# Performance work log

Hardware: AMD Instinct MI355X
Metric: run time of the kernel (lower is better)

The kernel has to match this reference:

```python
import jax, jax.numpy as jnp
import numpy as np

N_NODES = 100000
DROP_P = 0.2


def _degree_norm(idx, n):
    deg = jax.ops.segment_sum(jnp.ones_like(idx, dtype=jnp.float32), idx, num_segments=n)
    return jnp.maximum(deg, 1.0) ** -0.5


def gcn_layer(x, src, dst, W, b, n):
    # DGL GraphConv, norm='both', in_feats > out_feats so weight is applied first.
    norm_src = _degree_norm(src, n)  # out-degree^{-1/2}
    norm_dst = _degree_norm(dst, n)  # in-degree^{-1/2}
    h = (x * norm_src[:, None]) @ W            # [N, d_out]
    agg = jax.ops.segment_sum(h[src], dst, num_segments=n)  # gather-scatter over edges
    return agg * norm_dst[:, None] + b


def setup_inputs() -> dict:
    key = jax.random.key(0)
    k = jax.random.split(key, 5)
    x = jax.random.normal(k[0], (N_NODES, 256), dtype=jnp.float32)
    edge_index = jax.random.randint(k[1], (2, 1600000), 0, N_NODES, dtype=jnp.int64)
    W1 = jax.random.normal(k[2], (256, 128), dtype=jnp.float32) * (1.0 / np.sqrt(256))
    b1 = jnp.zeros((128,), dtype=jnp.float32)
    W2 = jax.random.normal(k[3], (128, 47), dtype=jnp.float32) * (1.0 / np.sqrt(128))
    b2 = jnp.zeros((47,), dtype=jnp.float32)
    return {"x": x, "edge_index": edge_index, "W1": W1, "b1": b1, "W2": W2, "b2": b2}


def reference(x, edge_index, W1, b1, W2, b2):
    src, dst = edge_index[0], edge_index[1]
    n = x.shape[0]
    # CRD: GraphConv -> relu -> dropout (F.dropout default training=True; fixed mask)
    h = gcn_layer(x, src, dst, W1, b1, n)
    h = jax.nn.relu(h)
    keep = jax.random.bernoulli(jax.random.key(42), 1.0 - DROP_P, h.shape)
    h = jnp.where(keep, h / (1.0 - DROP_P), 0.0)
    # CLS: GraphConv -> log_softmax over class dim
    out = gcn_layer(h, src, dst, W2, b2, n)
    return jax.nn.log_softmax(out, axis=-1)
```

## Files before the change

### kernel.cpp

```cpp
#include <hip/hip_runtime.h>
#include <math.h>


#define NF0 256
#define NF1 128
#define NC  47
#define CB  1024

typedef __attribute__((ext_vector_type(8))) short bfrag;
typedef __attribute__((ext_vector_type(4))) float f32x4;

__device__ __forceinline__ unsigned short f2bf(float f) {
  unsigned u = __float_as_uint(f);
  return (unsigned short)((u + 0x7fffu + ((u >> 16) & 1u)) >> 16);
}
__device__ __forceinline__ unsigned pack2bf(float a, float b) {
  return (unsigned)f2bf(a) | ((unsigned)f2bf(b) << 16);
}
__device__ __forceinline__ float bflo(unsigned v) { return __uint_as_float(v << 16); }
__device__ __forceinline__ float bfhi(unsigned v) { return __uint_as_float(v & 0xffff0000u); }
__device__ __forceinline__ float bf2f(unsigned short b) {
  return __uint_as_float((unsigned)b << 16);
}

__device__ __forceinline__ unsigned rotl_(unsigned x, int n) {
  return (x << n) | (x >> (32 - n));
}
__device__ __forceinline__ void threefry2x32_(unsigned x0, unsigned x1,
                                              unsigned& o0, unsigned& o1) {
  const unsigned k0 = 0u, k1 = 42u;
  const unsigned k2 = k0 ^ k1 ^ 0x1BD11BDAu;
  x0 += k0; x1 += k1;
  x0+=x1; x1=rotl_(x1,13); x1^=x0;
  x0+=x1; x1=rotl_(x1,15); x1^=x0;
  x0+=x1; x1=rotl_(x1,26); x1^=x0;
  x0+=x1; x1=rotl_(x1, 6); x1^=x0;
  x0+=k1; x1+=k2+1u;
  x0+=x1; x1=rotl_(x1,17); x1^=x0;
  x0+=x1; x1=rotl_(x1,29); x1^=x0;
  x0+=x1; x1=rotl_(x1,16); x1^=x0;
  x0+=x1; x1=rotl_(x1,24); x1^=x0;
  x0+=k2; x1+=k0+2u;
  x0+=x1; x1=rotl_(x1,13); x1^=x0;
  x0+=x1; x1=rotl_(x1,15); x1^=x0;
  x0+=x1; x1=rotl_(x1,26); x1^=x0;
  x0+=x1; x1=rotl_(x1, 6); x1^=x0;
  x0+=k0; x1+=k1+3u;
  x0+=x1; x1=rotl_(x1,17); x1^=x0;
  x0+=x1; x1=rotl_(x1,29); x1^=x0;
  x0+=x1; x1=rotl_(x1,16); x1^=x0;
  x0+=x1; x1=rotl_(x1,24); x1^=x0;
  x0+=k1; x1+=k2+4u;
  x0+=x1; x1=rotl_(x1,13); x1^=x0;
  x0+=x1; x1=rotl_(x1,15); x1^=x0;
  x0+=x1; x1=rotl_(x1,26); x1^=x0;
  x0+=x1; x1=rotl_(x1, 6); x1^=x0;
  x0+=k2; x1+=k0+5u;
  o0 = x0; o1 = x1;
}
__device__ __forceinline__ unsigned dropout_bit(unsigned j) {
  unsigned o0, o1;
  threefry2x32_(0u, j, o0, o1);
  unsigned bits = o0 ^ o1;
  float u = __uint_as_float((bits >> 9) | 0x3f800000u) - 1.0f;
  return (u < 0.8f) ? 1u : 0u;
}


__global__ __launch_bounds__(256) void k_chist(const int* __restrict__ ei, int E,
                                               int nbk,
                                               unsigned* __restrict__ bCntD,
                                               unsigned* __restrict__ bCntS,
                                               const float* __restrict__ W1,
                                               const float* __restrict__ W2,
                                               unsigned* __restrict__ W1t32,
                                               unsigned* __restrict__ W2t32) {
  if (blockIdx.x >= 256) {
    int i = (blockIdx.x - 256) * 256 + threadIdx.x;
    if (i < 128 * 128) {
      int n = i >> 7, k = (i & 127) << 1;
      W1t32[i] = pack2bf(W1[(size_t)k * NF1 + n], W1[(size_t)(k + 1) * NF1 + n]);
    } else if (i < 128 * 128 + 48 * 64) {
      int j = i - 128 * 128;
      int f = j >> 6, k = (j & 63) << 1;
      float a = (f < NC) ? W2[(size_t)k * NC + f] : 0.f;
      float c = (f < NC) ? W2[(size_t)(k + 1) * NC + f] : 0.f;
      W2t32[j] = pack2bf(a, c);
    }
    return;
  }
  __shared__ unsigned hd[128], hs[128];
  for (int i = threadIdx.x; i < 128; i += 256) { hd[i] = 0; hs[i] = 0; }
  __syncthreads();
  for (int e = blockIdx.x * 256 + threadIdx.x; e < E; e += 256 * 256) {
    int s = ei[e], d = ei[E + e];
    atomicAdd(&hs[s >> 10], 1u);
    atomicAdd(&hd[d >> 10], 1u);
  }
  __syncthreads();
  for (int i = threadIdx.x; i < nbk; i += 256) {
    if (hd[i]) atomicAdd(&bCntD[i], hd[i]);
    if (hs[i]) atomicAdd(&bCntS[i], hs[i]);
  }
}

__global__ __launch_bounds__(256) void k_cscatter(const int* __restrict__ ei, int E,
                                                  const unsigned* __restrict__ bCntD,
                                                  const unsigned* __restrict__ bCntS,
                                                  unsigned* __restrict__ curD,
                                                  unsigned* __restrict__ curS,
                                                  unsigned* __restrict__ pd,
                                                  unsigned short* __restrict__ ps,
                                                  int nbk) {
  __shared__ unsigned hd[128], hs[128];
  __shared__ unsigned baseD[128], baseS[128];
  __shared__ unsigned sc[256];
  const int t = threadIdx.x;
  int per = (E + gridDim.x - 1) / gridDim.x;
  int e0 = blockIdx.x * per;
  int e1 = min(e0 + per, E);
  unsigned orig = (t < 128) ? ((t < nbk) ? bCntD[t] : 0u)
                            : (((t - 128) < nbk) ? bCntS[t - 128] : 0u);
  sc[t] = orig;
  if (t < 128) { hd[t] = 0; hs[t] = 0; }
  __syncthreads();
  for (int e = e0 + t; e < e1; e += 256) {
    int s = ei[e], d = ei[E + e];
    atomicAdd(&hs[s >> 10], 1u);
    atomicAdd(&hd[d >> 10], 1u);
  }
  __syncthreads();
  #pragma unroll
  for (int o = 1; o < 128; o <<= 1) {
    unsigned u = ((t & 127) >= o) ? sc[t - o] : 0u;
    __syncthreads();
    sc[t] += u;
    __syncthreads();
  }
  if (t < 128) {
    unsigned excl = sc[t] - orig;
    unsigned h = hd[t];
    baseD[t] = excl + (h ? atomicAdd(&curD[t], h) : 0u);
    hd[t] = 0;
  } else {
    int i = t - 128;
    unsigned excl = sc[t] - orig;
    unsigned h = hs[i];
    baseS[i] = excl + (h ? atomicAdd(&curS[i], h) : 0u);
    hs[i] = 0;
  }
  __syncthreads();
  for (int e = e0 + t; e < e1; e += 256) {
    int s = ei[e], d = ei[E + e];
    int bd = d >> 10, bs = s >> 10;
    unsigned pD = baseD[bd] + atomicAdd(&hd[bd], 1u);
    unsigned pS = baseS[bs] + atomicAdd(&hs[bs], 1u);
    pd[pD] = ((unsigned)(d & (CB - 1)) << 17) | (unsigned)s;
    ps[pS] = (unsigned short)(s & (CB - 1));
  }
}

__global__ __launch_bounds__(256) void k_fine(const unsigned* __restrict__ bCntD,
                                              const unsigned* __restrict__ bCntS,
                                              const unsigned* __restrict__ pd,
                                              const unsigned short* __restrict__ ps,
                                              unsigned* __restrict__ off,
                                              float* __restrict__ norm_dst,
                                              float* __restrict__ norm_src,
                                              int* __restrict__ csr,
                                              int N, int E, int nbk,
                                              unsigned* __restrict__ bmask) {
  const int t = threadIdx.x;
  if ((int)blockIdx.x >= 2 * nbk) {
    int i = ((int)blockIdx.x - 2 * nbk) * 256 + t;
    if (i < 4 * N) {
      unsigned w = 0;
      #pragma unroll 4
      for (int tbit = 0; tbit < 32; tbit++)
        w |= dropout_bit(32u * (unsigned)i + (unsigned)tbit) << tbit;
      bmask[i] = w;
    }
    return;
  }
  __shared__ unsigned cnt[CB];
  __shared__ unsigned part[256];
  __shared__ unsigned sc[256];
  const bool isD = (int)blockIdx.x < nbk;
  const int b = isD ? (int)blockIdx.x : ((int)blockIdx.x - nbk);
  unsigned orig = (t < 128) ? ((t < nbk) ? bCntD[t] : 0u)
                            : (((t - 128) < nbk) ? bCntS[t - 128] : 0u);
  sc[t] = orig;
  __syncthreads();
  #pragma unroll
  for (int o = 1; o < 128; o <<= 1) {
    unsigned u = ((t & 127) >= o) ? sc[t - o] : 0u;
    __syncthreads();
    sc[t] += u;
    __syncthreads();
  }
  const int idx = isD ? b : (128 + b);
  const unsigned hi = sc[idx];
  const unsigned lo = hi - (isD ? bCntD[b] : bCntS[b]);
  const int base = b << 10;
  for (int i = t; i < CB; i += 256) cnt[i] = 0;
  __syncthreads();
  if (isD) {
    for (unsigned j = lo + t; j < hi; j += 256) atomicAdd(&cnt[pd[j] >> 17], 1u);
    __syncthreads();
    unsigned c0 = cnt[4*t], c1 = cnt[4*t+1], c2 = cnt[4*t+2], c3 = cnt[4*t+3];
    unsigned tsum = c0 + c1 + c2 + c3;
    part[t] = tsum;
    __syncthreads();
    #pragma unroll
    for (int o = 1; o < 256; o <<= 1) {
      unsigned u = (t >= o) ? part[t - o] : 0u;
      __syncthreads();
      part[t] += u;
      __syncthreads();
    }
    unsigned e0 = part[t] - tsum;
    unsigned p0 = e0, p1 = e0 + c0, p2 = p1 + c1, p3 = p2 + c2;
    int n0 = base + 4 * t;
    if (n0 + 0 < N) { off[n0+0] = lo + p0; norm_dst[n0+0] = 1.0f / sqrtf((float)(c0 < 1u ? 1u : c0)); }
    if (n0 + 1 < N) { off[n0+1] = lo + p1; norm_dst[n0+1] = 1.0f / sqrtf((float)(c1 < 1u ? 1u : c1)); }
    if (n0 + 2 < N) { off[n0+2] = lo + p2; norm_dst[n0+2] = 1.0f / sqrtf((float)(c2 < 1u ? 1u : c2)); }
    if (n0 + 3 < N) { off[n0+3] = lo + p3; norm_dst[n0+3] = 1.0f / sqrtf((float)(c3 < 1u ? 1u : c3)); }
    if (b == nbk - 1 && t == 0) off[N] = (unsigned)E;
    __syncthreads();
    cnt[4*t] = p0; cnt[4*t+1] = p1; cnt[4*t+2] = p2; cnt[4*t+3] = p3;
    __syncthreads();
    for (unsigned j = lo + t; j < hi; j += 256) {
      unsigned v = pd[j];
      unsigned pos = atomicAdd(&cnt[v >> 17], 1u);
      csr[lo + pos] = (int)(v & 0x1FFFFu);
    }
  } else {
    for (unsigned j = lo + t; j < hi; j += 256) atomicAdd(&cnt[ps[j]], 1u);
    __syncthreads();
    for (int i = t; i < CB; i += 256) {
      int n = base + i;
      if (n < N) {
        unsigned c = cnt[i];
        norm_src[n] = 1.0f / sqrtf((float)(c < 1u ? 1u : c));
      }
    }
  }
}

__global__ __launch_bounds__(256) void k_gemm1(const float* __restrict__ x,
                                               const unsigned* __restrict__ W1t32,
                                               const float* __restrict__ norm_src,
                                               unsigned short* __restrict__ h1, int N) {
  __shared__ unsigned As[128][20];
  __shared__ unsigned Bs[128][20];
  const int m0 = blockIdx.x * 128;
  const int t = threadIdx.x;
  const int lane = t & 63, wid = t >> 6;
  const int fr = lane & 15, ko = (lane >> 4) * 8;

  f32x4 acc[2][8];
  #pragma unroll
  for (int r = 0; r < 2; r++)
    #pragma unroll
    for (int c = 0; c < 8; c++) acc[r][c] = (f32x4){0.f, 0.f, 0.f, 0.f};

  const int sr = t >> 1;
  const int shw = (t & 1) * 8;

  for (int k0 = 0; k0 < NF0; k0 += 32) {
    {
      unsigned w[8];
      int gm = m0 + sr;
      if (gm < N) {
        const float* p = x + (size_t)gm * NF0 + k0 + shw * 2;
        #pragma unroll
        for (int q = 0; q < 4; q++) {
          float4 v = *(const float4*)(p + q * 4);
          w[2*q]   = pack2bf(v.x, v.y);
          w[2*q+1] = pack2bf(v.z, v.w);
        }
      } else {
        #pragma unroll
        for (int q = 0; q < 8; q++) w[q] = 0u;
      }
      *(uint4*)&As[sr][shw]     = make_uint4(w[0], w[1], w[2], w[3]);
      *(uint4*)&As[sr][shw + 4] = make_uint4(w[4], w[5], w[6], w[7]);
    }
    {
      const unsigned* pb = W1t32 + (size_t)sr * (NF0 / 2) + (k0 >> 1) + shw;
      *(uint4*)&Bs[sr][shw]     = *(const uint4*)pb;
      *(uint4*)&Bs[sr][shw + 4] = *(const uint4*)(pb + 4);
    }
    __syncthreads();
    const unsigned short* As16 = (const unsigned short*)&As[0][0];
    const unsigned short* Bs16 = (const unsigned short*)&Bs[0][0];
    #pragma unroll
    for (int r = 0; r < 2; r++) {
      bfrag a = *(const bfrag*)(As16 + (size_t)(wid * 32 + r * 16 + fr) * 40 + ko);
      #pragma unroll
      for (int c = 0; c < 8; c++) {
        bfrag b = *(const bfrag*)(Bs16 + (size_t)(c * 16 + fr) * 40 + ko);
        acc[r][c] = __builtin_amdgcn_mfma_f32_16x16x32_bf16(a, b, acc[r][c], 0, 0, 0);
      }
    }
    __syncthreads();
  }

  #pragma unroll
  for (int r = 0; r < 2; r++) {
    int rbase = m0 + wid * 32 + r * 16 + (lane >> 4) * 4;
    float ns[4];
    #pragma unroll
    for (int g = 0; g < 4; g++) ns[g] = (rbase + g < N) ? norm_src[rbase + g] : 0.f;
    #pragma unroll
    for (int c = 0; c < 8; c++) {
      int col = c * 16 + fr;
      #pragma unroll
      for (int g = 0; g < 4; g++) {
        int row = rbase + g;
        if (row < N) h1[(size_t)row * NF1 + col] = f2bf(acc[r][c][g] * ns[g]);
      }
    }
  }
}

__global__ __launch_bounds__(256) void k_gather1(const unsigned* __restrict__ off,
                                                 const int* __restrict__ csr,
                                                 const unsigned short* __restrict__ h1,
                                                 const float* __restrict__ norm_dst,
                                                 const float* __restrict__ norm_src,
                                                 const float* __restrict__ b1,
                                                 const unsigned* __restrict__ bmask,
                                                 const unsigned* __restrict__ W2t32,
                                                 unsigned short* __restrict__ g64,
                                                 int N) {
  const int t = threadIdx.x;
  const int lane = t & 63, wid = t >> 6;
  const int eg = lane >> 4;
  const int q  = lane & 15;
  const float4 bA = *(const float4*)(b1 + q * 8);
  const float4 bB = *(const float4*)(b1 + q * 8 + 4);

  const int wbase = (blockIdx.x * 4 + wid) * 16;
  if (wbase >= N) return;

  uint4 af[4];
  #pragma unroll
  for (int kk = 0; kk < 4; kk++) af[kk] = make_uint4(0u, 0u, 0u, 0u);

  #pragma unroll 1
  for (int i = 0; i < 16; i++) {
    const int node = wbase + i;
    if (node >= N) break;
    unsigned j = off[node], e1 = off[node + 1];
    float ax0=0.f, ax1=0.f, ax2=0.f, ax3=0.f;
    float ay0=0.f, ay1=0.f, ay2=0.f, ay3=0.f;
    for (; j + 8 <= e1; j += 8) {
      int sA = csr[j + eg];
      int sB = csr[j + 4 + eg];
      uint4 vA = *(const uint4*)(h1 + (size_t)sA * NF1 + q * 8);
      uint4 vB = *(const uint4*)(h1 + (size_t)sB * NF1 + q * 8);
      ax0 += bflo(vA.x) + bflo(vB.x); ay0 += bfhi(vA.x) + bfhi(vB.x);
      ax1 += bflo(vA.y) + bflo(vB.y); ay1 += bfhi(vA.y) + bfhi(vB.y);
      ax2 += bflo(vA.z) + bflo(vB.z); ay2 += bfhi(vA.z) + bfhi(vB.z);
      ax3 += bflo(vA.w) + bflo(vB.w); ay3 += bfhi(vA.w) + bfhi(vB.w);
    }
    if (j + 4 <= e1) {
      int s = csr[j + eg];
      uint4 v = *(const uint4*)(h1 + (size_t)s * NF1 + q * 8);
      ax0 += bflo(v.x); ay0 += bfhi(v.x);
      ax1 += bflo(v.y); ay1 += bfhi(v.y);
      ax2 += bflo(v.z); ay2 += bfhi(v.z);
      ax3 += bflo(v.w); ay3 += bfhi(v.w);
      j += 4;
    }
    if (j < e1) {
      unsigned rem = e1 - j;
      if ((unsigned)eg < rem) {
        int s = csr[j + eg];
        uint4 v = *(const uint4*)(h1 + (size_t)s * NF1 + q * 8);
        ax0 += bflo(v.x); ay0 += bfhi(v.x);
        ax1 += bflo(v.y); ay1 += bfhi(v.y);
        ax2 += bflo(v.z); ay2 += bfhi(v.z);
        ax3 += bflo(v.w); ay3 += bfhi(v.w);
      }
    }
    ax0 += __shfl_xor(ax0, 16); ax0 += __shfl_xor(ax0, 32);
    ay0 += __shfl_xor(ay0, 16); ay0 += __shfl_xor(ay0, 32);
    ax1 += __shfl_xor(ax1, 16); ax1 += __shfl_xor(ax1, 32);
    ay1 += __shfl_xor(ay1, 16); ay1 += __shfl_xor(ay1, 32);
    ax2 += __shfl_xor(ax2, 16); ax2 += __shfl_xor(ax2, 32);
    ay2 += __shfl_xor(ay2, 16); ay2 += __shfl_xor(ay2, 32);
    ax3 += __shfl_xor(ax3, 16); ax3 += __shfl_xor(ax3, 32);
    ay3 += __shfl_xor(ay3, 16); ay3 += __shfl_xor(ay3, 32);
    float nd = norm_dst[node], ns = norm_src[node];
    unsigned mw = bmask[node * 4 + (q >> 2)];
    unsigned mb = (mw >> ((q & 3) * 8)) & 0xffu;
    float v0 = fmaxf(ax0 * nd + bA.x, 0.f);
    float v1 = fmaxf(ay0 * nd + bA.y, 0.f);
    float v2 = fmaxf(ax1 * nd + bA.z, 0.f);
    float v3 = fmaxf(ay1 * nd + bA.w, 0.f);
    float v4 = fmaxf(ax2 * nd + bB.x, 0.f);
    float v5 = fmaxf(ay2 * nd + bB.y, 0.f);
    float v6 = fmaxf(ax3 * nd + bB.z, 0.f);
    float v7 = fmaxf(ay3 * nd + bB.w, 0.f);
    v0 *= ((mb >> 0) & 1 ? 1.25f : 0.f) * ns;
    v1 *= ((mb >> 1) & 1 ? 1.25f : 0.f) * ns;
    v2 *= ((mb >> 2) & 1 ? 1.25f : 0.f) * ns;
    v3 *= ((mb >> 3) & 1 ? 1.25f : 0.f) * ns;
    v4 *= ((mb >> 4) & 1 ? 1.25f : 0.f) * ns;
    v5 *= ((mb >> 5) & 1 ? 1.25f : 0.f) * ns;
    v6 *= ((mb >> 6) & 1 ? 1.25f : 0.f) * ns;
    v7 *= ((mb >> 7) & 1 ? 1.25f : 0.f) * ns;
    uint4 o;
    o.x = pack2bf(v0, v1);
    o.y = pack2bf(v2, v3);
    o.z = pack2bf(v4, v5);
    o.w = pack2bf(v6, v7);
    #pragma unroll
    for (int kk = 0; kk < 4; kk++) {
      int srcl = 4 * kk + eg;
      unsigned t0 = __shfl(o.x, srcl);
      unsigned t1 = __shfl(o.y, srcl);
      unsigned t2 = __shfl(o.z, srcl);
      unsigned t3 = __shfl(o.w, srcl);
      if (q == i) af[kk] = make_uint4(t0, t1, t2, t3);
    }
  }

  #pragma unroll
  for (int c = 0; c < 3; c++) {
    f32x4 acc = (f32x4){0.f, 0.f, 0.f, 0.f};
    const unsigned* bp = W2t32 + (size_t)(c * 16 + q) * 64 + eg * 4;
    #pragma unroll
    for (int kk = 0; kk < 4; kk++) {
      uint4 w = *(const uint4*)(bp + kk * 16);
      acc = __builtin_amdgcn_mfma_f32_16x16x32_bf16(*(bfrag*)&af[kk], *(bfrag*)&w,
                                                    acc, 0, 0, 0);
    }
    int col = c * 16 + q;
    #pragma unroll
    for (int r = 0; r < 4; r++) {
      int nr = wbase + eg * 4 + r;
      if (nr < N) g64[(size_t)nr * 64 + col] = f2bf(acc[r]);
    }
  }
  #pragma unroll
  for (int r = 0; r < 4; r++) {
    int nr = wbase + eg * 4 + r;
    if (nr < N) g64[(size_t)nr * 64 + 48 + q] = 0;
  }
}

__global__ __launch_bounds__(256) void k_gather2(const unsigned* __restrict__ off,
                                                 const int* __restrict__ csr,
                                                 const unsigned* __restrict__ g64,
                                                 const float* __restrict__ norm_dst,
                                                 const float* __restrict__ b2,
                                                 float* __restrict__ out, int N) {
  int node = (blockIdx.x * 256 + threadIdx.x) >> 6;
  int lane = threadIdx.x & 63;
  if (node >= N) return;
  const int h = lane >> 5, q = lane & 31;
  unsigned j = off[node], e1 = off[node + 1];
  float a0 = 0.f, a1 = 0.f;
  for (; j + 8 <= e1; j += 8) {
    int s0 = csr[j + h],     s1 = csr[j + 2 + h];
    int s2 = csr[j + 4 + h], s3 = csr[j + 6 + h];
    unsigned v0 = g64[(size_t)s0 * 32 + q];
    unsigned v1 = g64[(size_t)s1 * 32 + q];
    unsigned v2 = g64[(size_t)s2 * 32 + q];
    unsigned v3 = g64[(size_t)s3 * 32 + q];
    a0 += (bflo(v0) + bflo(v1)) + (bflo(v2) + bflo(v3));
    a1 += (bfhi(v0) + bfhi(v1)) + (bfhi(v2) + bfhi(v3));
  }
  if (j + 4 <= e1) {
    int sA = csr[j + h], sB = csr[j + 2 + h];
    unsigned vA = g64[(size_t)sA * 32 + q];
    unsigned vB = g64[(size_t)sB * 32 + q];
    a0 += bflo(vA) + bflo(vB);
    a1 += bfhi(vA) + bfhi(vB);
    j += 4;
  }
  if (j + 2 <= e1) {
    int s = csr[j + h];
    unsigned v = g64[(size_t)s * 32 + q];
    a0 += bflo(v); a1 += bfhi(v);
    j += 2;
  }
  if (j < e1 && h == 0) {
    int s = csr[j];
    unsigned v = g64[(size_t)s * 32 + q];
    a0 += bflo(v); a1 += bfhi(v);
  }
  a0 += __shfl_xor(a0, 32);
  a1 += __shfl_xor(a1, 32);
  float nd = norm_dst[node];
  int f0 = 2 * q, f1 = 2 * q + 1;
  float v0 = (f0 < NC) ? a0 * nd + b2[f0] : -INFINITY;
  float v1 = (f1 < NC) ? a1 * nd + b2[f1] : -INFINITY;
  float m = fmaxf(v0, v1);
  #pragma unroll
  for (int o = 16; o; o >>= 1) m = fmaxf(m, __shfl_xor(m, o));
  float ex = ((f0 < NC) ? expf(v0 - m) : 0.f) + ((f1 < NC) ? expf(v1 - m) : 0.f);
  #pragma unroll
  for (int o = 16; o; o >>= 1) ex += __shfl_xor(ex, o);
  float ls = logf(ex);
  if (h == 0) {
    if (f0 < NC) out[(size_t)node * NC + f0] = v0 - m - ls;
    if (f1 < NC) out[(size_t)node * NC + f1] = v1 - m - ls;
  }
}

extern "C" void kernel_launch(void* const* d_in, const int* in_sizes, int n_in,
                              void* d_out, int out_size, void* d_ws, size_t ws_size,
                              hipStream_t stream) {
  const float* x  = (const float*)d_in[0];
  const int*   ei = (const int*)d_in[1];
  const float* W1 = (const float*)d_in[2];
  const float* b1 = (const float*)d_in[3];
  const float* W2 = (const float*)d_in[4];
  const float* b2 = (const float*)d_in[5];
  float* out = (float*)d_out;

  const int N = in_sizes[0] / NF0;
  const int E = in_sizes[1] / 2;
  const int nbk = (N + CB - 1) / CB;
  const int Npad = (N + 63) & ~63;

  unsigned* ws = (unsigned*)d_ws;
  size_t o = 0;
  auto alloc = [&](size_t elems) { size_t p = o; o += (elems + 3) & ~(size_t)3; return p; };
  float*    norm_src = (float*)(ws + alloc(N));
  float*    norm_dst = (float*)(ws + alloc(N));
  unsigned* off      = ws + alloc(N + 1);
  unsigned* bCntD    = ws + alloc(128);
  unsigned* bCntS    = ws + alloc(128);
  unsigned* curD     = ws + alloc(128);
  unsigned* curS     = ws + alloc(128);
  unsigned* bmask    = ws + alloc((size_t)4 * N);
  unsigned* pd       = ws + alloc(E);
  unsigned short* ps = (unsigned short*)(ws + alloc(E / 2));
  int*      csr      = (int*)(ws + alloc(E));
  unsigned* W1t32    = ws + alloc(128 * 128);
  unsigned* W2t32    = ws + alloc(48 * 64);
  unsigned short* h1 = (unsigned short*)(ws + alloc((size_t)N * NF1 / 2));
  unsigned* g64u     = ws + alloc((size_t)Npad * 32);
  unsigned short* g64 = (unsigned short*)g64u;

  hipMemsetAsync(bCntD, 0, 512 * sizeof(unsigned), stream);

  int wblk = (128 * 128 + 48 * 64 + 255) / 256;
  int mblk = (4 * N + 255) / 256;
  k_chist<<<256 + wblk, 256, 0, stream>>>(ei, E, nbk, bCntD, bCntS, W1, W2,
                                          W1t32, W2t32);
  k_cscatter<<<256, 256, 0, stream>>>(ei, E, bCntD, bCntS, curD, curS, pd, ps, nbk);
  k_fine<<<2 * nbk + mblk, 256, 0, stream>>>(bCntD, bCntS, pd, ps, off, norm_dst,
                                             norm_src, csr, N, E, nbk, bmask);
  k_gemm1<<<(N + 127) / 128, 256, 0, stream>>>(x, W1t32, norm_src, h1, N);
  k_gather1<<<(N + 63) / 64, 256, 0, stream>>>(off, csr, h1, norm_dst, norm_src,
                                               b1, bmask, W2t32, g64, N);
  k_gather2<<<((size_t)N * 64 + 255) / 256, 256, 0, stream>>>(
      off, csr, (const unsigned*)g64u, norm_dst, b2, out, N);
}
```

Measured before the change: 436.2 us.

## Count source degrees directly and fuse scatter, GEMM and dropout mask into one kernel

Source out-degree is now counted per node with global atomics in the histogram kernel. This removes the source-side bucket scatter and the fine-pass work that existed only to compute norm_src, and the ps array is dropped. The coarse dst scatter, the first GEMM and the dropout-mask generation now run as independent block ranges of one launched kernel. k_fine only handles the dst CSR, with one fewer launch overall. The trade-off is 1.6M global atomics on the source counter array and recomputing rsqrt in the GEMM epilogue and in gather1.

```diff
diff --git a/kernel.cpp b/kernel.cpp
--- a/kernel.cpp
+++ b/kernel.cpp
@@ -66,11 +66,10 @@
   return (u < 0.8f) ? 1u : 0u;
 }
 
-
 __global__ __launch_bounds__(256) void k_chist(const int* __restrict__ ei, int E,
                                                int nbk,
                                                unsigned* __restrict__ bCntD,
-                                               unsigned* __restrict__ bCntS,
+                                               unsigned* __restrict__ srcCnt,
                                                const float* __restrict__ W1,
                                                const float* __restrict__ W2,
                                                unsigned* __restrict__ W1t32,
@@ -89,238 +88,222 @@
     }
     return;
   }
-  __shared__ unsigned hd[128], hs[128];
-  for (int i = threadIdx.x; i < 128; i += 256) { hd[i] = 0; hs[i] = 0; }
+  __shared__ unsigned hd[128];
+  for (int i = threadIdx.x; i < 128; i += 256) hd[i] = 0;
   __syncthreads();
   for (int e = blockIdx.x * 256 + threadIdx.x; e < E; e += 256 * 256) {
     int s = ei[e], d = ei[E + e];
-    atomicAdd(&hs[s >> 10], 1u);
+    atomicAdd(&srcCnt[s], 1u);
     atomicAdd(&hd[d >> 10], 1u);
   }
   __syncthreads();
   for (int i = threadIdx.x; i < nbk; i += 256) {
     if (hd[i]) atomicAdd(&bCntD[i], hd[i]);
-    if (hs[i]) atomicAdd(&bCntS[i], hs[i]);
-  }
-}
-
-__global__ __launch_bounds__(256) void k_cscatter(const int* __restrict__ ei, int E,
-                                                  const unsigned* __restrict__ bCntD,
-                                                  const unsigned* __restrict__ bCntS,
-                                                  unsigned* __restrict__ curD,
-                                                  unsigned* __restrict__ curS,
-                                                  unsigned* __restrict__ pd,
-                                                  unsigned short* __restrict__ ps,
-                                                  int nbk) {
-  __shared__ unsigned hd[128], hs[128];
-  __shared__ unsigned baseD[128], baseS[128];
-  __shared__ unsigned sc[256];
+  }
+}
+
+__global__ __launch_bounds__(256) void k_super(const int* __restrict__ ei, int E,
+                                               int nbk, int N, int gblk,
+                                               const unsigned* __restrict__ bCntD,
+                                               unsigned* __restrict__ curD,
+                                               unsigned* __restrict__ pd,
+                                               const float* __restrict__ x,
+                                               const unsigned* __restrict__ W1t32,
+                                               const unsigned* __restrict__ srcCnt,
+                                               unsigned short* __restrict__ h1,
+                                               unsigned* __restrict__ bmask) {
+  __shared__ unsigned smem[2 * 128 * 20];
   const int t = threadIdx.x;
-  int per = (E + gridDim.x - 1) / gridDim.x;
-  int e0 = blockIdx.x * per;
-  int e1 = min(e0 + per, E);
-  unsigned orig = (t < 128) ? ((t < nbk) ? bCntD[t] : 0u)
-                            : (((t - 128) < nbk) ? bCntS[t - 128] : 0u);
-  sc[t] = orig;
-  if (t < 128) { hd[t] = 0; hs[t] = 0; }
-  __syncthreads();
-  for (int e = e0 + t; e < e1; e += 256) {
-    int s = ei[e], d = ei[E + e];
-    atomicAdd(&hs[s >> 10], 1u);
-    atomicAdd(&hd[d >> 10], 1u);
-  }
-  __syncthreads();
-  #pragma unroll
-  for (int o = 1; o < 128; o <<= 1) {
-    unsigned u = ((t & 127) >= o) ? sc[t - o] : 0u;
-    __syncthreads();
-    sc[t] += u;
-    __syncthreads();
-  }
-  if (t < 128) {
-    unsigned excl = sc[t] - orig;
-    unsigned h = hd[t];
-    baseD[t] = excl + (h ? atomicAdd(&curD[t], h) : 0u);
-    hd[t] = 0;
-  } else {
-    int i = t - 128;
-    unsigned excl = sc[t] - orig;
-    unsigned h = hs[i];
-    baseS[i] = excl + (h ? atomicAdd(&curS[i], h) : 0u);
-    hs[i] = 0;
-  }
-  __syncthreads();
-  for (int e = e0 + t; e < e1; e += 256) {
-    int s = ei[e], d = ei[E + e];
-    int bd = d >> 10, bs = s >> 10;
-    unsigned pD = baseD[bd] + atomicAdd(&hd[bd], 1u);
-    unsigned pS = baseS[bs] + atomicAdd(&hs[bs], 1u);
-    pd[pD] = ((unsigned)(d & (CB - 1)) << 17) | (unsigned)s;
-    ps[pS] = (unsigned short)(s & (CB - 1));
-  }
-}
-
-__global__ __launch_bounds__(256) void k_fine(const unsigned* __restrict__ bCntD,
-                                              const unsigned* __restrict__ bCntS,
-                                              const unsigned* __restrict__ pd,
-                                              const unsigned short* __restrict__ ps,
-                                              unsigned* __restrict__ off,
-                                              float* __restrict__ norm_dst,
-                                              float* __restrict__ norm_src,
-                                              int* __restrict__ csr,
-                                              int N, int E, int nbk,
-                                              unsigned* __restrict__ bmask) {
-  const int t = threadIdx.x;
-  if ((int)blockIdx.x >= 2 * nbk) {
-    int i = ((int)blockIdx.x - 2 * nbk) * 256 + t;
-    if (i < 4 * N) {
-      unsigned w = 0;
-      #pragma unroll 4
-      for (int tbit = 0; tbit < 32; tbit++)
-        w |= dropout_bit(32u * (unsigned)i + (unsigned)tbit) << tbit;
-      bmask[i] = w;
+
+  if ((int)blockIdx.x < 256) {
+    unsigned* hd    = smem;
+    unsigned* baseD = smem + 128;
+    unsigned* sc    = smem + 256;
+    const int per = (E + 255) / 256;
+    const int e0 = blockIdx.x * per;
+    const int e1 = min(e0 + per, E);
+    unsigned orig = 0;
+    if (t < 128) {
+      orig = (t < nbk) ? bCntD[t] : 0u;
+      sc[t] = orig;
+      hd[t] = 0;
+    }
+    __syncthreads();
+    for (int e = e0 + t; e < e1; e += 256) {
+      int d = ei[E + e];
+      atomicAdd(&hd[d >> 10], 1u);
+    }
+    __syncthreads();
+    #pragma unroll
+    for (int o = 1; o < 128; o <<= 1) {
+      unsigned u = (t < 128 && t >= o) ? sc[t - o] : 0u;
+      __syncthreads();
+      if (t < 128) sc[t] += u;
+      __syncthreads();
+    }
+    if (t < 128) {
+      unsigned excl = sc[t] - orig;
+      unsigned h = hd[t];
+      baseD[t] = excl + (h ? atomicAdd(&curD[t], h) : 0u);
+      hd[t] = 0;
+    }
+    __syncthreads();
+    for (int e = e0 + t; e < e1; e += 256) {
+      int s = ei[e], d = ei[E + e];
+      int bd = d >> 10;
+      unsigned pD = baseD[bd] + atomicAdd(&hd[bd], 1u);
+      pd[pD] = ((unsigned)(d & (CB - 1)) << 17) | (unsigned)s;
     }
     return;
   }
-  __shared__ unsigned cnt[CB];
-  __shared__ unsigned part[256];
-  __shared__ unsigned sc[256];
-  const bool isD = (int)blockIdx.x < nbk;
-  const int b = isD ? (int)blockIdx.x : ((int)blockIdx.x - nbk);
-  unsigned orig = (t < 128) ? ((t < nbk) ? bCntD[t] : 0u)
-                            : (((t - 128) < nbk) ? bCntS[t - 128] : 0u);
-  sc[t] = orig;
-  __syncthreads();
-  #pragma unroll
-  for (int o = 1; o < 128; o <<= 1) {
-    unsigned u = ((t & 127) >= o) ? sc[t - o] : 0u;
-    __syncthreads();
-    sc[t] += u;
-    __syncthreads();
-  }
-  const int idx = isD ? b : (128 + b);
-  const unsigned hi = sc[idx];
-  const unsigned lo = hi - (isD ? bCntD[b] : bCntS[b]);
-  const int base = b << 10;
-  for (int i = t; i < CB; i += 256) cnt[i] = 0;
-  __syncthreads();
-  if (isD) {
-    for (unsigned j = lo + t; j < hi; j += 256) atomicAdd(&cnt[pd[j] >> 17], 1u);
-    __syncthreads();
-    unsigned c0 = cnt[4*t], c1 = cnt[4*t+1], c2 = cnt[4*t+2], c3 = cnt[4*t+3];
-    unsigned tsum = c0 + c1 + c2 + c3;
-    part[t] = tsum;
-    __syncthreads();
+
+  if ((int)blockIdx.x < 256 + gblk) {
+    unsigned (*As)[20] = (unsigned(*)[20])smem;
+    unsigned (*Bs)[20] = (unsigned(*)[20])(smem + 128 * 20);
+    const int m0 = ((int)blockIdx.x - 256) * 128;
+    const int lane = t & 63, wid = t >> 6;
+    const int fr = lane & 15, ko = (lane >> 4) * 8;
+
+    f32x4 acc[2][8];
     #pragma unroll
-    for (int o = 1; o < 256; o <<= 1) {
-      unsigned u = (t >= o) ? part[t - o] : 0u;
+    for (int r = 0; r < 2; r++)
+      #pragma unroll
+      for (int c = 0; c < 8; c++) acc[r][c] = (f32x4){0.f, 0.f, 0.f, 0.f};
+
+    const int sr = t >> 1;
+    const int shw = (t & 1) * 8;
+
+    for (int k0 = 0; k0 < NF0; k0 += 32) {
+      {
+        unsigned w[8];
+        int gm = m0 + sr;
+        if (gm < N) {
+          const float* p = x + (size_t)gm * NF0 + k0 + shw * 2;
+          #pragma unroll
+          for (int q = 0; q < 4; q++) {
+            float4 v = *(const float4*)(p + q * 4);
+            w[2*q]   = pack2bf(v.x, v.y);
+            w[2*q+1] = pack2bf(v.z, v.w);
+          }
+        } else {
+          #pragma unroll
+          for (int q = 0; q < 8; q++) w[q] = 0u;
+        }
+        *(uint4*)&As[sr][shw]     = make_uint4(w[0], w[1], w[2], w[3]);
+        *(uint4*)&As[sr][shw + 4] = make_uint4(w[4], w[5], w[6], w[7]);
+      }
+      {
+        const unsigned* pb = W1t32 + (size_t)sr * (NF0 / 2) + (k0 >> 1) + shw;
+        *(uint4*)&Bs[sr][shw]     = *(const uint4*)pb;
+        *(uint4*)&Bs[sr][shw + 4] = *(const uint4*)(pb + 4);
+      }
       __syncthreads();
-      part[t] += u;
+      const unsigned short* As16 = (const unsigned short*)smem;
+      const unsigned short* Bs16 = (const unsigned short*)(smem + 128 * 20);
+      #pragma unroll
+      for (int r = 0; r < 2; r++) {
+        bfrag a = *(const bfrag*)(As16 + (size_t)(wid * 32 + r * 16 + fr) * 40 + ko);
+        #pragma unroll
+        for (int c = 0; c < 8; c++) {
+          bfrag b = *(const bfrag*)(Bs16 + (size_t)(c * 16 + fr) * 40 + ko);
+          acc[r][c] = __builtin_amdgcn_mfma_f32_16x16x32_bf16(a, b, acc[r][c], 0, 0, 0);
+        }
+      }
       __syncthreads();
     }
-    unsigned e0 = part[t] - tsum;
-    unsigned p0 = e0, p1 = e0 + c0, p2 = p1 + c1, p3 = p2 + c2;
-    int n0 = base + 4 * t;
-    if (n0 + 0 < N) { off[n0+0] = lo + p0; norm_dst[n0+0] = 1.0f / sqrtf((float)(c0 < 1u ? 1u : c0)); }
-    if (n0 + 1 < N) { off[n0+1] = lo + p1; norm_dst[n0+1] = 1.0f / sqrtf((float)(c1 < 1u ? 1u : c1)); }
-    if (n0 + 2 < N) { off[n0+2] = lo + p2; norm_dst[n0+2] = 1.0f / sqrtf((float)(c2 < 1u ? 1u : c2)); }
-    if (n0 + 3 < N) { off[n0+3] = lo + p3; norm_dst[n0+3] = 1.0f / sqrtf((float)(c3 < 1u ? 1u : c3)); }
-    if (b == nbk - 1 && t == 0) off[N] = (unsigned)E;
-    __syncthreads();
-    cnt[4*t] = p0; cnt[4*t+1] = p1; cnt[4*t+2] = p2; cnt[4*t+3] = p3;
-    __syncthreads();
-    for (unsigned j = lo + t; j < hi; j += 256) {
-      unsigned v = pd[j];
-      unsigned pos = atomicAdd(&cnt[v >> 17], 1u);
-      csr[lo + pos] = (int)(v & 0x1FFFFu);
-    }
-  } else {
-    for (unsigned j = lo + t; j < hi; j += 256) atomicAdd(&cnt[ps[j]], 1u);
-    __syncthreads();
-    for (int i = t; i < CB; i += 256) {
-      int n = base + i;
-      if (n < N) {
-        unsigned c = cnt[i];
-        norm_src[n] = 1.0f / sqrtf((float)(c < 1u ? 1u : c));
-      }
-    }
-  }
-}
-
-__global__ __launch_bounds__(256) void k_gemm1(const float* __restrict__ x,
-                                               const unsigned* __restrict__ W1t32,
-                                               const float* __restrict__ norm_src,
-                                               unsigned short* __restrict__ h1, int N) {
-  __shared__ unsigned As[128][20];
-  __shared__ unsigned Bs[128][20];
-  const int m0 = blockIdx.x * 128;
-  const int t = threadIdx.x;
-  const int lane = t & 63, wid = t >> 6;
-  const int fr = lane & 15, ko = (lane >> 4) * 8;
-
-  f32x4 acc[2][8];
-  #pragma unroll
-  for (int r = 0; r < 2; r++)
-    #pragma unroll
-    for (int c = 0; c < 8; c++) acc[r][c] = (f32x4){0.f, 0.f, 0.f, 0.f};
-
-  const int sr = t >> 1;
-  const int shw = (t & 1) * 8;
-
-  for (int k0 = 0; k0 < NF0; k0 += 32) {
-    {
-      unsigned w[8];
-      int gm = m0 + sr;
-      if (gm < N) {
-        const float* p = x + (size_t)gm * NF0 + k0 + shw * 2;
-        #pragma unroll
-        for (int q = 0; q < 4; q++) {
-          float4 v = *(const float4*)(p + q * 4);
-          w[2*q]   = pack2bf(v.x, v.y);
-          w[2*q+1] = pack2bf(v.z, v.w);
-        }
-      } else {
-        #pragma unroll
-        for (int q = 0; q < 8; q++) w[q] = 0u;
-      }
-      *(uint4*)&As[sr][shw]     = make_uint4(w[0], w[1], w[2], w[3]);
-      *(uint4*)&As[sr][shw + 4] = make_uint4(w[4], w[5], w[6], w[7]);
-    }
-    {
-      const unsigned* pb = W1t32 + (size_t)sr * (NF0 / 2) + (k0 >> 1) + shw;
-      *(uint4*)&Bs[sr][shw]     = *(const uint4*)pb;
-      *(uint4*)&Bs[sr][shw + 4] = *(const uint4*)(pb + 4);
-    }
-    __syncthreads();
-    const unsigned short* As16 = (const unsigned short*)&As[0][0];
-    const unsigned short* Bs16 = (const unsigned short*)&Bs[0][0];
+
     #pragma unroll
     for (int r = 0; r < 2; r++) {
-      bfrag a = *(const bfrag*)(As16 + (size_t)(wid * 32 + r * 16 + fr) * 40 + ko);
-      #pragma unroll
-      for (int c = 0; c < 8; c++) {
-        bfrag b = *(const bfrag*)(Bs16 + (size_t)(c * 16 + fr) * 40 + ko);
-        acc[r][c] = __builtin_amdgcn_mfma_f32_16x16x32_bf16(a, b, acc[r][c], 0, 0, 0);
-      }
-    }
-    __syncthreads();
-  }
-
-  #pragma unroll
-  for (int r = 0; r < 2; r++) {
-    int rbase = m0 + wid * 32 + r * 16 + (lane >> 4) * 4;
-    float ns[4];
-    #pragma unroll
-    for (int g = 0; g < 4; g++) ns[g] = (rbase + g < N) ? norm_src[rbase + g] : 0.f;
-    #pragma unroll
-    for (int c = 0; c < 8; c++) {
-      int col = c * 16 + fr;
+      int rbase = m0 + wid * 32 + r * 16 + (lane >> 4) * 4;
+      float ns[4];
       #pragma unroll
       for (int g = 0; g < 4; g++) {
         int row = rbase + g;
-        if (row < N) h1[(size_t)row * NF1 + col] = f2bf(acc[r][c][g] * ns[g]);
+        if (row < N) {
+          unsigned c = srcCnt[row];
+          ns[g] = 1.0f / sqrtf((float)(c < 1u ? 1u : c));
+        } else ns[g] = 0.f;
       }
-    }
+      #pragma unroll
+      for (int c = 0; c < 8; c++) {
+        int col = c * 16 + fr;
+        #pragma unroll
+        for (int g = 0; g < 4; g++) {
+          int row = rbase + g;
+          if (row < N) h1[(size_t)row * NF1 + col] = f2bf(acc[r][c][g] * ns[g]);
+        }
+      }
+    }
+    return;
+  }
+
+  int i = ((int)blockIdx.x - 256 - gblk) * 256 + t;
+  if (i < 4 * N) {
+    unsigned w = 0;
+    #pragma unroll 4
+    for (int tbit = 0; tbit < 32; tbit++)
+      w |= dropout_bit(32u * (unsigned)i + (unsigned)tbit) << tbit;
+    bmask[i] = w;
+  }
+}
+
+__global__ __launch_bounds__(256) void k_fine(const unsigned* __restrict__ bCntD,
+                                              const unsigned* __restrict__ pd,
+                                              unsigned* __restrict__ off,
+                                              float* __restrict__ norm_dst,
+                                              int* __restrict__ csr,
+                                              int N, int E, int nbk) {
+  __shared__ unsigned cnt[CB];
+  __shared__ unsigned part[256];
+  __shared__ unsigned sc[128];
+  const int t = threadIdx.x;
+  const int b = blockIdx.x;
+  unsigned orig = 0;
+  if (t < 128) {
+    orig = (t < nbk) ? bCntD[t] : 0u;
+    sc[t] = orig;
+  }
+  __syncthreads();
+  #pragma unroll
+  for (int o = 1; o < 128; o <<= 1) {
+    unsigned u = (t < 128 && t >= o) ? sc[t - o] : 0u;
+    __syncthreads();
+    if (t < 128) sc[t] += u;
+    __syncthreads();
+  }
+  const unsigned hi = sc[b];
+  const unsigned lo = hi - bCntD[b];
+  const int base = b << 10;
+  for (int i = t; i < CB; i += 256) cnt[i] = 0;
+  __syncthreads();
+  for (unsigned j = lo + t; j < hi; j += 256) atomicAdd(&cnt[pd[j] >> 17], 1u);
+  __syncthreads();
+  unsigned c0 = cnt[4*t], c1 = cnt[4*t+1], c2 = cnt[4*t+2], c3 = cnt[4*t+3];
+  unsigned tsum = c0 + c1 + c2 + c3;
+  part[t] = tsum;
+  __syncthreads();
+  #pragma unroll
+  for (int o = 1; o < 256; o <<= 1) {
+    unsigned u = (t >= o) ? part[t - o] : 0u;
+    __syncthreads();
+    part[t] += u;
+    __syncthreads();
+  }
+  unsigned e0 = part[t] - tsum;
+  unsigned p0 = e0, p1 = e0 + c0, p2 = p1 + c1, p3 = p2 + c2;
+  int n0 = base + 4 * t;
+  if (n0 + 0 < N) { off[n0+0] = lo + p0; norm_dst[n0+0] = 1.0f / sqrtf((float)(c0 < 1u ? 1u : c0)); }
+  if (n0 + 1 < N) { off[n0+1] = lo + p1; norm_dst[n0+1] = 1.0f / sqrtf((float)(c1 < 1u ? 1u : c1)); }
+  if (n0 + 2 < N) { off[n0+2] = lo + p2; norm_dst[n0+2] = 1.0f / sqrtf((float)(c2 < 1u ? 1u : c2)); }
+  if (n0 + 3 < N) { off[n0+3] = lo + p3; norm_dst[n0+3] = 1.0f / sqrtf((float)(c3 < 1u ? 1u : c3)); }
+  if (b == nbk - 1 && t == 0) off[N] = (unsigned)E;
+  __syncthreads();
+  cnt[4*t] = p0; cnt[4*t+1] = p1; cnt[4*t+2] = p2; cnt[4*t+3] = p3;
+  __syncthreads();
+  for (unsigned j = lo + t; j < hi; j += 256) {
+    unsigned v = pd[j];
+    unsigned pos = atomicAdd(&cnt[v >> 17], 1u);
+    csr[lo + pos] = (int)(v & 0x1FFFFu);
   }
 }
 
@@ -328,7 +311,7 @@
                                                  const int* __restrict__ csr,
                                                  const unsigned short* __restrict__ h1,
                                                  const float* __restrict__ norm_dst,
-                                                 const float* __restrict__ norm_src,
+                                                 const unsigned* __restrict__ srcCnt,
                                                  const float* __restrict__ b1,
                                                  const unsigned* __restrict__ bmask,
                                                  const unsigned* __restrict__ W2t32,
@@ -393,7 +376,9 @@
     ay2 += __shfl_xor(ay2, 16); ay2 += __shfl_xor(ay2, 32);
     ax3 += __shfl_xor(ax3, 16); ax3 += __shfl_xor(ax3, 32);
     ay3 += __shfl_xor(ay3, 16); ay3 += __shfl_xor(ay3, 32);
-    float nd = norm_dst[node], ns = norm_src[node];
+    float nd = norm_dst[node];
+    unsigned sc = srcCnt[node];
+    float ns = 1.0f / sqrtf((float)(sc < 1u ? 1u : sc));
     unsigned mw = bmask[node * 4 + (q >> 2)];
     unsigned mb = (mw >> ((q & 3) * 8)) & 0xffu;
     float v0 = fmaxf(ax0 * nd + bA.x, 0.f);
@@ -531,16 +516,13 @@
   unsigned* ws = (unsigned*)d_ws;
   size_t o = 0;
   auto alloc = [&](size_t elems) { size_t p = o; o += (elems + 3) & ~(size_t)3; return p; };
-  float*    norm_src = (float*)(ws + alloc(N));
   float*    norm_dst = (float*)(ws + alloc(N));
   unsigned* off      = ws + alloc(N + 1);
   unsigned* bCntD    = ws + alloc(128);
-  unsigned* bCntS    = ws + alloc(128);
   unsigned* curD     = ws + alloc(128);
-  unsigned* curS     = ws + alloc(128);
+  unsigned* srcCnt   = ws + alloc(N);
   unsigned* bmask    = ws + alloc((size_t)4 * N);
   unsigned* pd       = ws + alloc(E);
-  unsigned short* ps = (unsigned short*)(ws + alloc(E / 2));
   int*      csr      = (int*)(ws + alloc(E));
   unsigned* W1t32    = ws + alloc(128 * 128);
   unsigned* W2t32    = ws + alloc(48 * 64);
@@ -548,17 +530,17 @@
   unsigned* g64u     = ws + alloc((size_t)Npad * 32);
   unsigned short* g64 = (unsigned short*)g64u;
 
-  hipMemsetAsync(bCntD, 0, 512 * sizeof(unsigned), stream);
+  hipMemsetAsync(bCntD, 0, (size_t)(256 + N) * sizeof(unsigned), stream);
 
   int wblk = (128 * 128 + 48 * 64 + 255) / 256;
+  int gblk = (N + 127) / 128;
   int mblk = (4 * N + 255) / 256;
-  k_chist<<<256 + wblk, 256, 0, stream>>>(ei, E, nbk, bCntD, bCntS, W1, W2,
+  k_chist<<<256 + wblk, 256, 0, stream>>>(ei, E, nbk, bCntD, srcCnt, W1, W2,
                                           W1t32, W2t32);
-  k_cscatter<<<256, 256, 0, stream>>>(ei, E, bCntD, bCntS, curD, curS, pd, ps, nbk);
-  k_fine<<<2 * nbk + mblk, 256, 0, stream>>>(bCntD, bCntS, pd, ps, off, norm_dst,
-                                             norm_src, csr, N, E, nbk, bmask);
-  k_gemm1<<<(N + 127) / 128, 256, 0, stream>>>(x, W1t32, norm_src, h1, N);
-  k_gather1<<<(N + 63) / 64, 256, 0, stream>>>(off, csr, h1, norm_dst, norm_src,
+  k_super<<<256 + gblk + mblk, 256, 0, stream>>>(ei, E, nbk, N, gblk, bCntD, curD,
+                                                 pd, x, W1t32, srcCnt, h1, bmask);
+  k_fine<<<nbk, 256, 0, stream>>>(bCntD, pd, off, norm_dst, csr, N, E, nbk);
+  k_gather1<<<(N + 63) / 64, 256, 0, stream>>>(off, csr, h1, norm_dst, srcCnt,
                                                b1, bmask, W2t32, g64, N);
   k_gather2<<<((size_t)N * 64 + 255) / 256, 256, 0, stream>>>(
       off, csr, (const unsigned*)g64u, norm_dst, b2, out, N);
```

Result: slower. 472.7 us (+8.4%).
